# Performance work log

Measured on AMD Instinct MI355X. Metric: run time of the kernel, lower is better.

The kernel has to match this reference:

```python
import jax, jax.numpy as jnp
import numpy as np

B, T, C = 4, 2048, 1024
N_HEAD = 16
HEAD_DIM = C // N_HEAD


def setup_inputs() -> dict:
    key = jax.random.key(0)
    k1, k2, k3 = jax.random.split(key, 3)
    x = jax.random.normal(k1, (B, T, C), dtype=jnp.float32)
    # Linear weights stored as (in, out); scaled like typical init
    w_qkv = jax.random.normal(k2, (C, 3 * C), dtype=jnp.float32) * (1.0 / np.sqrt(C))
    w_proj = jax.random.normal(k3, (C, C), dtype=jnp.float32) * (1.0 / np.sqrt(C))
    return {"x": x, "w_qkv": w_qkv, "w_proj": w_proj}


def reference(x, w_qkv, w_proj):
    b, t, c = x.shape
    qkv = x @ w_qkv                      # (B,T,3C)
    q, k, v = jnp.split(qkv, 3, axis=-1)
    # (B,H,T,D)
    def to_heads(a):
        return a.reshape(b, t, N_HEAD, HEAD_DIM).transpose(0, 2, 1, 3)
    q, k, v = to_heads(q), to_heads(k), to_heads(v)
    scale = 1.0 / np.sqrt(HEAD_DIM).astype(np.float32)
    att = jnp.einsum('bhqd,bhkd->bhqk', q, k) * scale   # (B,H,T,T)
    causal = jnp.tril(jnp.ones((t, t), dtype=bool))
    att = jnp.where(causal[None, None, :, :], att, -jnp.inf)
    att = jax.nn.softmax(att, axis=-1)
    # dropout p=0.0 (eval) -> identity
    y = jnp.einsum('bhqk,bhkd->bhqd', att, v)            # (B,H,T,D)
    y = y.transpose(0, 2, 1, 3).reshape(b, t, c)
    return y @ w_proj
```

## Files before the change

### kernel.cpp

```cpp
#include <hip/hip_runtime.h>
#include <hip/hip_bf16.h>
#include <stdint.h>

#define Bsz 4
#define Tsz 2048
#define Csz 1024
#define Hn  16
#define Dh  64
#define BH  (Bsz*Hn)
#define Mrows (Bsz*Tsz)
#define N1  (3*Csz)

typedef short s16x8 __attribute__((ext_vector_type(8)));
typedef short s16x4 __attribute__((ext_vector_type(4)));
typedef float fx4   __attribute__((ext_vector_type(4)));

static __device__ __forceinline__ short f2bf(float x) {
  __hip_bfloat16 h = __float2bfloat16(x);
  return __builtin_bit_cast(short, h);
}

#define GLDS16(g, l) __builtin_amdgcn_global_load_lds( \
    (const __attribute__((address_space(1))) void*)(g), \
    (__attribute__((address_space(3))) void*)(l), 16, 0, 0)

__global__ void cvt_kernel(const float* __restrict__ in, short* __restrict__ out, int n4) {
  int i = blockIdx.x * blockDim.x + threadIdx.x;
  int stride = blockDim.x * gridDim.x;
  for (; i < n4; i += stride) {
    float4 v = ((const float4*)in)[i];
    s16x4 o;
    o.x = f2bf(v.x); o.y = f2bf(v.y); o.z = f2bf(v.z); o.w = f2bf(v.w);
    ((s16x4*)out)[i] = o;
  }
}

__global__ void transpose_cvt_kernel(const float* __restrict__ w, short* __restrict__ wt,
                                     int K, int N) {
  __shared__ float tile[32][33];
  int tc = threadIdx.x & 31;
  int tr = threadIdx.x >> 5;
  int n0 = blockIdx.x * 32;
  int k0 = blockIdx.y * 32;
#pragma unroll
  for (int p = 0; p < 4; p++) {
    int r = tr + p*8;
    tile[r][tc] = w[(size_t)(k0 + r) * N + (n0 + tc)];
  }
  __syncthreads();
#pragma unroll
  for (int p = 0; p < 4; p++) {
    int r = tr + p*8;
    wt[(size_t)(n0 + r) * K + (k0 + tc)] = f2bf(tile[tc][r]);
  }
}

static __device__ __forceinline__ void gemm_stage(
    const short* __restrict__ Ab, const short* __restrict__ Bb, int Kdim, int k0,
    short* __restrict__ sA, short* __restrict__ sB, int tid)
{
#pragma unroll
  for (int i = 0; i < 2; i++) {
    int c  = tid + 256*i;
    int mr = c >> 3;
    int l  = (c & 7) ^ (mr & 7);
    int row = mr*2 + (l >> 2);
    int ko  = (l & 3) * 8;
    GLDS16(Ab + (size_t)row * Kdim + k0 + ko, sA + c*8);
    GLDS16(Bb + (size_t)row * Kdim + k0 + ko, sB + c*8);
  }
}

static __device__ __forceinline__ void gemm_compute(
    const short* __restrict__ sA, const short* __restrict__ sB,
    int m_off, int n_off, int lr, int lq, fx4 acc[4][4])
{
  s16x8 af[4], bf[4];
#pragma unroll
  for (int mt = 0; mt < 4; mt++) {
    int m = m_off + mt*16 + lr, mr = m >> 1;
    int p = (((m & 1)*4 + lq)) ^ (mr & 7);
    af[mt] = *(const s16x8*)(sA + mr*64 + p*8);
  }
#pragma unroll
  for (int nt = 0; nt < 4; nt++) {
    int n = n_off + nt*16 + lr, nr = n >> 1;
    int p = (((n & 1)*4 + lq)) ^ (nr & 7);
    bf[nt] = *(const s16x8*)(sB + nr*64 + p*8);
  }
#pragma unroll
  for (int mt = 0; mt < 4; mt++)
#pragma unroll
    for (int nt = 0; nt < 4; nt++)
      acc[mt][nt] = __builtin_amdgcn_mfma_f32_16x16x32_bf16(af[mt], bf[nt], acc[mt][nt], 0, 0, 0);
}

__global__ __launch_bounds__(256) void gemm_bt_kernel(
    const short* __restrict__ A, const short* __restrict__ Bt,
    float* __restrict__ Cf,
    short* __restrict__ Qo, short* __restrict__ Ko, short* __restrict__ Vo,
    int Mdim, int Ndim, int Kdim, int mode)
{
  __shared__ __align__(16) short sA[2][128*32];
  __shared__ __align__(16) short sB[2][128*32];
  const int tid  = threadIdx.x;
  const int lane = tid & 63;
  const int lr   = lane & 15;
  const int lq   = lane >> 4;
  const int wv   = tid >> 6;
  const int nb   = Ndim >> 7;
  const int bm   = (int)blockIdx.x / nb;
  const int bn   = (int)blockIdx.x % nb;
  const int m_off = (wv & 1) << 6;
  const int n_off = (wv >> 1) << 6;

  const short* Ab = A  + (size_t)bm * 128 * Kdim;
  const short* Bb = Bt + (size_t)bn * 128 * Kdim;

  fx4 acc[4][4];
#pragma unroll
  for (int i = 0; i < 4; i++)
#pragma unroll
    for (int j = 0; j < 4; j++) acc[i][j] = (fx4){0.f, 0.f, 0.f, 0.f};

  const int NIT = Kdim >> 5;
  gemm_stage(Ab, Bb, Kdim, 0, sA[0], sB[0], tid);
  for (int it = 0; it < NIT; it += 2) {
    __syncthreads();
    if (it + 1 < NIT) gemm_stage(Ab, Bb, Kdim, (it+1)*32, sA[1], sB[1], tid);
    gemm_compute(sA[0], sB[0], m_off, n_off, lr, lq, acc);
    __syncthreads();
    if (it + 2 < NIT) gemm_stage(Ab, Bb, Kdim, (it+2)*32, sA[0], sB[0], tid);
    gemm_compute(sA[1], sB[1], m_off, n_off, lr, lq, acc);
  }

  const int gm0 = bm*128 + m_off;
  const int gn0 = bn*128 + n_off;
  if (mode == 0) {
#pragma unroll
    for (int mt = 0; mt < 4; mt++)
#pragma unroll
      for (int nt = 0; nt < 4; nt++) {
        int col = gn0 + nt*16 + lr;
#pragma unroll
        for (int r = 0; r < 4; r++) {
          int row = gm0 + mt*16 + lq*4 + r;
          Cf[(size_t)row * Ndim + col] = acc[mt][nt][r];
        }
      }
  } else {
#pragma unroll
    for (int mt = 0; mt < 4; mt++)
#pragma unroll
      for (int nt = 0; nt < 4; nt++) {
        int n   = gn0 + nt*16 + lr;
        int sec = n >> 10;
        int cc  = n & 1023;
        int hh  = cc >> 6;
        int dd  = cc & 63;
        if (sec == 2) {
          int tt0 = gm0 + mt*16 + lq*4;
          int bb  = tt0 >> 11;
          int bh  = bb * Hn + hh;
          s16x4 pk;
          pk.x = f2bf(acc[mt][nt][0]); pk.y = f2bf(acc[mt][nt][1]);
          pk.z = f2bf(acc[mt][nt][2]); pk.w = f2bf(acc[mt][nt][3]);
          *(s16x4*)(Vo + ((size_t)bh * Dh + dd) * Tsz + (tt0 & 2047)) = pk;
        } else {
#pragma unroll
          for (int r = 0; r < 4; r++) {
            int m  = gm0 + mt*16 + lq*4 + r;
            int bb = m >> 11;
            int tt = m & 2047;
            int bh = bb * Hn + hh;
            short v = f2bf(acc[mt][nt][r]);
            if (sec == 0) Qo[((size_t)bh * Tsz + tt) * Dh + dd] = v;
            else          Ko[((size_t)bh * Tsz + tt) * Dh + dd] = v;
          }
        }
      }
  }
}

#define PPITCH 72

static __device__ __forceinline__ void attn_stage(
    const short* __restrict__ Kp, const short* __restrict__ Vp, int kbase,
    short* __restrict__ sK, short* __restrict__ sV,
    int c0, int r0, int g0, int c1, int r1, int g1)
{
  GLDS16(Kp + (size_t)(kbase + r0)*Dh + g0, sK + c0*8);
  GLDS16(Kp + (size_t)(kbase + r1)*Dh + g1, sK + c1*8);
  GLDS16(Vp + (size_t)r0*Tsz + kbase + g0, sV + c0*8);
  GLDS16(Vp + (size_t)r1*Tsz + kbase + g1, sV + c1*8);
}

static __device__ __forceinline__ void attn_compute(
    const short* __restrict__ sK, const short* __restrict__ sV,
    int kbase, int q0, int lr, int lq, int sw,
    short* __restrict__ pb, const s16x8 bq[2][2], fx4 o[2][4], float li[2])
{
  const float sc = 0.125f * 1.44269504f;
  const bool masked = (kbase + 63 > q0);

  fx4 s[2][4];
#pragma unroll
  for (int j = 0; j < 2; j++)
#pragma unroll
    for (int mt = 0; mt < 4; mt++) s[j][mt] = (fx4){0.f,0.f,0.f,0.f};
#pragma unroll
  for (int mt = 0; mt < 4; mt++)
#pragma unroll
    for (int kk = 0; kk < 2; kk++) {
      const s16x8 akf = *(const s16x8*)(sK + (mt*16 + lr)*64 + ((kk*4 + lq) ^ sw)*8);
      s[0][mt] = __builtin_amdgcn_mfma_f32_16x16x32_bf16(akf, bq[0][kk], s[0][mt], 0, 0, 0);
      s[1][mt] = __builtin_amdgcn_mfma_f32_16x16x32_bf16(akf, bq[1][kk], s[1][mt], 0, 0, 0);
    }

#pragma unroll
  for (int j = 0; j < 2; j++) {
    const int qg = q0 + 16*j + lr;
    float p[16];
#pragma unroll
    for (int mt = 0; mt < 4; mt++)
#pragma unroll
      for (int r = 0; r < 4; r++) {
        float v = s[j][mt][r];
        if (masked) {
          int jg = kbase + mt*16 + lq*4 + r;
          v = (jg <= qg) ? v : -1e30f;
        }
        p[mt*4 + r] = __builtin_amdgcn_exp2f(v * sc);
      }
    float s8[8];
#pragma unroll
    for (int i = 0; i < 8; i++) s8[i] = p[i] + p[i+8];
    float s4[4];
#pragma unroll
    for (int i = 0; i < 4; i++) s4[i] = s8[i] + s8[i+4];
    li[j] += (s4[0] + s4[2]) + (s4[1] + s4[3]);
#pragma unroll
    for (int mt = 0; mt < 4; mt++) {
      s16x4 pk;
      pk.x = f2bf(p[mt*4+0]); pk.y = f2bf(p[mt*4+1]);
      pk.z = f2bf(p[mt*4+2]); pk.w = f2bf(p[mt*4+3]);
      *(s16x4*)(pb + (16*j + lr)*PPITCH + mt*16 + lq*4) = pk;
    }
  }
  __asm__ __volatile__("" ::: "memory");
  s16x8 pf[2][2];
#pragma unroll
  for (int j = 0; j < 2; j++)
#pragma unroll
    for (int kk = 0; kk < 2; kk++)
      pf[j][kk] = *(const s16x8*)(pb + (16*j + lr)*PPITCH + kk*32 + lq*8);
  __asm__ __volatile__("" ::: "memory");

#pragma unroll
  for (int dt = 0; dt < 4; dt++)
#pragma unroll
    for (int kk = 0; kk < 2; kk++) {
      const s16x8 avf = *(const s16x8*)(sV + (dt*16 + lr)*64 + ((kk*4 + lq) ^ sw)*8);
      o[0][dt] = __builtin_amdgcn_mfma_f32_16x16x32_bf16(avf, pf[0][kk], o[0][dt], 0, 0, 0);
      o[1][dt] = __builtin_amdgcn_mfma_f32_16x16x32_bf16(avf, pf[1][kk], o[1][dt], 0, 0, 0);
    }
}

__global__ __launch_bounds__(256) void attn_kernel(
    const short* __restrict__ Qb, const short* __restrict__ Kb,
    const short* __restrict__ Vt, short* __restrict__ Y)
{
  __shared__ __align__(16) short sK[2][64*64];
  __shared__ __align__(16) short sV[2][64*64];
  __shared__ __align__(16) short pbuf[4][32*PPITCH];
  const int tid  = threadIdx.x;
  const int lane = tid & 63;
  const int wv   = tid >> 6;
  const int lr   = lane & 15;
  const int lq   = lane >> 4;
  const int sw   = lr & 7;
  const int bh   = blockIdx.x;
  const int qb   = 15 - (int)blockIdx.y;
  const int b    = bh >> 4;
  const int h    = bh & 15;
  const int q0   = qb*128 + wv*32;

  const short* Qp = Qb + (size_t)bh * Tsz * Dh;
  const short* Kp = Kb + (size_t)bh * Tsz * Dh;
  const short* Vp = Vt + (size_t)bh * Dh * Tsz;
  short* pb = pbuf[wv];

  const int c0 = tid,       r0 = c0 >> 3, g0 = (((c0 & 7) ^ (r0 & 7)) * 8);
  const int c1 = tid + 256, r1 = c1 >> 3, g1 = (((c1 & 7) ^ (r1 & 7)) * 8);

  s16x8 bq[2][2];
#pragma unroll
  for (int j = 0; j < 2; j++)
#pragma unroll
    for (int kk = 0; kk < 2; kk++)
      bq[j][kk] = *(const s16x8*)(Qp + (size_t)(q0 + 16*j + lr)*Dh + kk*32 + lq*8);

  fx4 o[2][4];
#pragma unroll
  for (int j = 0; j < 2; j++)
#pragma unroll
    for (int i = 0; i < 4; i++) o[j][i] = (fx4){0.f, 0.f, 0.f, 0.f};
  float li[2] = {0.f, 0.f};

  const int ntiles = 2*qb + 2;
  attn_stage(Kp, Vp, 0, sK[0], sV[0], c0, r0, g0, c1, r1, g1);
  for (int kt = 0; kt < ntiles; kt += 2) {
    __syncthreads();
    if (kt + 1 < ntiles) attn_stage(Kp, Vp, (kt+1)*64, sK[1], sV[1], c0, r0, g0, c1, r1, g1);
    if (kt*64 <= q0 + 31)
      attn_compute(sK[0], sV[0], kt*64, q0, lr, lq, sw, pb, bq, o, li);
    __syncthreads();
    if (kt + 2 < ntiles) attn_stage(Kp, Vp, (kt+2)*64, sK[0], sV[0], c0, r0, g0, c1, r1, g1);
    if ((kt+1)*64 <= q0 + 31)
      attn_compute(sK[1], sV[1], (kt+1)*64, q0, lr, lq, sw, pb, bq, o, li);
  }

#pragma unroll
  for (int j = 0; j < 2; j++) {
    float l = li[j];
    l += __shfl_xor(l, 16);
    l += __shfl_xor(l, 32);
    float inv = 1.0f / l;
#pragma unroll
    for (int dt = 0; dt < 4; dt++) {
      s16x4 yk;
      yk.x = f2bf(o[j][dt][0]*inv); yk.y = f2bf(o[j][dt][1]*inv);
      yk.z = f2bf(o[j][dt][2]*inv); yk.w = f2bf(o[j][dt][3]*inv);
      *(s16x4*)(Y + ((size_t)b*Tsz + q0 + 16*j + lr)*Csz + h*Dh + dt*16 + lq*4) = yk;
    }
  }
}

extern "C" void kernel_launch(void* const* d_in, const int* in_sizes, int n_in,
                              void* d_out, int out_size, void* d_ws, size_t ws_size,
                              hipStream_t stream)
{
  const float* x  = (const float*)d_in[0];
  const float* wq = (const float*)d_in[1];
  const float* wp = (const float*)d_in[2];
  float* out = (float*)d_out;

  char* ws = (char*)d_ws;
  size_t off = 0;
  short* xb  = (short*)(ws + off); off += (size_t)Mrows*Csz*2;
  short* wqT = (short*)(ws + off); off += (size_t)N1*Csz*2;
  short* wpT = (short*)(ws + off); off += (size_t)Csz*Csz*2;
  short* Qb  = (short*)(ws + off); off += (size_t)BH*Tsz*Dh*2;
  short* Kb  = (short*)(ws + off); off += (size_t)BH*Tsz*Dh*2;
  short* Vt  = (short*)(ws + off); off += (size_t)BH*Dh*Tsz*2;
  short* Yb  = (short*)(ws + off); off += (size_t)Mrows*Csz*2;

  cvt_kernel<<<1024, 256, 0, stream>>>(x, xb, Mrows*Csz/4);
  transpose_cvt_kernel<<<dim3(N1/32, Csz/32), 256, 0, stream>>>(wq, wqT, Csz, N1);
  transpose_cvt_kernel<<<dim3(Csz/32, Csz/32), 256, 0, stream>>>(wp, wpT, Csz, Csz);
  gemm_bt_kernel<<<(Mrows/128)*(N1/128), 256, 0, stream>>>(
      xb, wqT, nullptr, Qb, Kb, Vt, Mrows, N1, Csz, 1);
  attn_kernel<<<dim3(BH, Tsz/128), 256, 0, stream>>>(Qb, Kb, Vt, Yb);
  gemm_bt_kernel<<<(Mrows/128)*(Csz/128), 256, 0, stream>>>(
      Yb, wpT, out, nullptr, nullptr, nullptr, Mrows, Csz, Csz, 0);
}
```

Before: 263.2 us.

## Restructure GEMM into 128x256 tiles with triple-buffered LDS pipeline

The bf16 GEMM now uses 512-thread blocks computing 128x256 output tiles with a K step of 64. LDS staging is triple-buffered, with explicit vmcnt waits so global->LDS loads for stage t+2 overlap the MFMAs of stage t. MFMA clusters are split into two halves separated by barriers and wrapped in s_setprio, and swizzled LDS offsets are precomputed once. This is meant to cut barrier and load latency and raise MFMA utilisation, at the cost of more LDS per block (144 KB), which lowers occupancy, and fewer blocks in the grid.

```diff
diff --git a/kernel.cpp b/kernel.cpp
--- a/kernel.cpp
+++ b/kernel.cpp
@@ -55,67 +55,55 @@
   }
 }
 
-static __device__ __forceinline__ void gemm_stage(
-    const short* __restrict__ Ab, const short* __restrict__ Bb, int Kdim, int k0,
-    short* __restrict__ sA, short* __restrict__ sB, int tid)
-{
-#pragma unroll
-  for (int i = 0; i < 2; i++) {
-    int c  = tid + 256*i;
-    int mr = c >> 3;
-    int l  = (c & 7) ^ (mr & 7);
-    int row = mr*2 + (l >> 2);
-    int ko  = (l & 3) * 8;
-    GLDS16(Ab + (size_t)row * Kdim + k0 + ko, sA + c*8);
-    GLDS16(Bb + (size_t)row * Kdim + k0 + ko, sB + c*8);
-  }
-}
-
-static __device__ __forceinline__ void gemm_compute(
-    const short* __restrict__ sA, const short* __restrict__ sB,
-    int m_off, int n_off, int lr, int lq, fx4 acc[4][4])
-{
-  s16x8 af[4], bf[4];
-#pragma unroll
-  for (int mt = 0; mt < 4; mt++) {
-    int m = m_off + mt*16 + lr, mr = m >> 1;
-    int p = (((m & 1)*4 + lq)) ^ (mr & 7);
-    af[mt] = *(const s16x8*)(sA + mr*64 + p*8);
-  }
-#pragma unroll
-  for (int nt = 0; nt < 4; nt++) {
-    int n = n_off + nt*16 + lr, nr = n >> 1;
-    int p = (((n & 1)*4 + lq)) ^ (nr & 7);
-    bf[nt] = *(const s16x8*)(sB + nr*64 + p*8);
-  }
-#pragma unroll
-  for (int mt = 0; mt < 4; mt++)
-#pragma unroll
-    for (int nt = 0; nt < 4; nt++)
-      acc[mt][nt] = __builtin_amdgcn_mfma_f32_16x16x32_bf16(af[mt], bf[nt], acc[mt][nt], 0, 0, 0);
-}
-
-__global__ __launch_bounds__(256) void gemm_bt_kernel(
+static __device__ __forceinline__ s16x8 lds_frag(const short* p, int off) {
+  return *(const s16x8*)(p + off);
+}
+
+__global__ __launch_bounds__(512) void gemm_bt_kernel(
     const short* __restrict__ A, const short* __restrict__ Bt,
     float* __restrict__ Cf,
     short* __restrict__ Qo, short* __restrict__ Ko, short* __restrict__ Vo,
     int Mdim, int Ndim, int Kdim, int mode)
 {
-  __shared__ __align__(16) short sA[2][128*32];
-  __shared__ __align__(16) short sB[2][128*32];
+  __shared__ __align__(16) short sA[3][128*64];
+  __shared__ __align__(16) short sB[3][256*64];
   const int tid  = threadIdx.x;
   const int lane = tid & 63;
   const int lr   = lane & 15;
   const int lq   = lane >> 4;
   const int wv   = tid >> 6;
-  const int nb   = Ndim >> 7;
+  const int nb   = Ndim >> 8;
   const int bm   = (int)blockIdx.x / nb;
   const int bn   = (int)blockIdx.x % nb;
   const int m_off = (wv & 1) << 6;
   const int n_off = (wv >> 1) << 6;
 
   const short* Ab = A  + (size_t)bm * 128 * Kdim;
-  const short* Bb = Bt + (size_t)bn * 128 * Kdim;
+  const short* Bb = Bt + (size_t)bn * 256 * Kdim;
+
+  const short* gA[2];
+  const short* gB[4];
+#pragma unroll
+  for (int j = 0; j < 2; j++) {
+    int c = tid + 512*j, r = c >> 3, o = ((c & 7) ^ (r & 7)) * 8;
+    gA[j] = Ab + (size_t)r * Kdim + o;
+  }
+#pragma unroll
+  for (int j = 0; j < 4; j++) {
+    int c = tid + 512*j, r = c >> 3, o = ((c & 7) ^ (r & 7)) * 8;
+    gB[j] = Bb + (size_t)r * Kdim + o;
+  }
+
+  int offA[4][2], offB[4][2];
+#pragma unroll
+  for (int ft = 0; ft < 4; ft++)
+#pragma unroll
+    for (int kk = 0; kk < 2; kk++) {
+      int ra = m_off + ft*16 + lr;
+      offA[ft][kk] = ra*64 + ((((kk<<2) | lq) ^ (ra & 7)) << 3);
+      int rb = n_off + ft*16 + lr;
+      offB[ft][kk] = rb*64 + ((((kk<<2) | lq) ^ (rb & 7)) << 3);
+    }
 
   fx4 acc[4][4];
 #pragma unroll
@@ -123,19 +111,82 @@
 #pragma unroll
     for (int j = 0; j < 4; j++) acc[i][j] = (fx4){0.f, 0.f, 0.f, 0.f};
 
-  const int NIT = Kdim >> 5;
-  gemm_stage(Ab, Bb, Kdim, 0, sA[0], sB[0], tid);
-  for (int it = 0; it < NIT; it += 2) {
-    __syncthreads();
-    if (it + 1 < NIT) gemm_stage(Ab, Bb, Kdim, (it+1)*32, sA[1], sB[1], tid);
-    gemm_compute(sA[0], sB[0], m_off, n_off, lr, lq, acc);
-    __syncthreads();
-    if (it + 2 < NIT) gemm_stage(Ab, Bb, Kdim, (it+2)*32, sA[0], sB[0], tid);
-    gemm_compute(sA[1], sB[1], m_off, n_off, lr, lq, acc);
+  auto STAGE = [&](int k0, short* dA, short* dB) {
+    GLDS16(gA[0] + k0, dA + tid*8);
+    GLDS16(gA[1] + k0, dA + (tid+512)*8);
+    GLDS16(gB[0] + k0, dB + tid*8);
+    GLDS16(gB[1] + k0, dB + (tid+512)*8);
+    GLDS16(gB[2] + k0, dB + (tid+1024)*8);
+    GLDS16(gB[3] + k0, dB + (tid+1536)*8);
+  };
+
+  const int NIT = Kdim >> 6;
+
+  STAGE(0,  sA[0], sB[0]);
+  STAGE(64, sA[1], sB[1]);
+  __asm__ __volatile__("s_waitcnt vmcnt(6)" ::: "memory");
+  __builtin_amdgcn_s_barrier();
+
+  const short *cA = sA[0], *cB = sB[0];
+  const short *nA = sA[1], *nB = sB[1];
+  short *eA = sA[2], *eB = sB[2];
+
+  for (int t = 0; t < NIT; ++t) {
+    if (t + 2 < NIT) STAGE((t+2)*64, eA, eB);
+
+    s16x8 af[4][2], bf[2][2];
+#pragma unroll
+    for (int mt = 0; mt < 4; mt++)
+#pragma unroll
+      for (int kk = 0; kk < 2; kk++)
+        af[mt][kk] = lds_frag(cA, offA[mt][kk]);
+#pragma unroll
+    for (int nt = 0; nt < 2; nt++)
+#pragma unroll
+      for (int kk = 0; kk < 2; kk++)
+        bf[nt][kk] = lds_frag(cB, offB[nt][kk]);
+    __builtin_amdgcn_s_setprio(1);
+#pragma unroll
+    for (int kk = 0; kk < 2; kk++)
+#pragma unroll
+      for (int mt = 0; mt < 4; mt++) {
+        acc[mt][0] = __builtin_amdgcn_mfma_f32_16x16x32_bf16(af[mt][kk], bf[0][kk], acc[mt][0], 0, 0, 0);
+        acc[mt][1] = __builtin_amdgcn_mfma_f32_16x16x32_bf16(af[mt][kk], bf[1][kk], acc[mt][1], 0, 0, 0);
+      }
+    __builtin_amdgcn_s_setprio(0);
+    __builtin_amdgcn_sched_barrier(0);
+    __builtin_amdgcn_s_barrier();
+
+#pragma unroll
+    for (int nt = 0; nt < 2; nt++)
+#pragma unroll
+      for (int kk = 0; kk < 2; kk++)
+        bf[nt][kk] = lds_frag(cB, offB[nt+2][kk]);
+    __builtin_amdgcn_s_setprio(1);
+#pragma unroll
+    for (int kk = 0; kk < 2; kk++)
+#pragma unroll
+      for (int mt = 0; mt < 4; mt++) {
+        acc[mt][2] = __builtin_amdgcn_mfma_f32_16x16x32_bf16(af[mt][kk], bf[0][kk], acc[mt][2], 0, 0, 0);
+        acc[mt][3] = __builtin_amdgcn_mfma_f32_16x16x32_bf16(af[mt][kk], bf[1][kk], acc[mt][3], 0, 0, 0);
+      }
+    __builtin_amdgcn_s_setprio(0);
+    __builtin_amdgcn_sched_barrier(0);
+    if (t + 2 < NIT) {
+      __asm__ __volatile__("s_waitcnt vmcnt(6)" ::: "memory");
+    } else if (t + 1 < NIT) {
+      __asm__ __volatile__("s_waitcnt vmcnt(0)" ::: "memory");
+    }
+    __builtin_amdgcn_s_barrier();
+
+    const short *tAp = cA, *tBp = cB;
+    cA = nA; cB = nB;
+    nA = eA; nB = eB;
+    eA = (short*)tAp; eB = (short*)tBp;
   }
 
   const int gm0 = bm*128 + m_off;
-  const int gn0 = bn*128 + n_off;
+  const int gn0 = bn*256 + n_off;
   if (mode == 0) {
 #pragma unroll
     for (int mt = 0; mt < 4; mt++)
@@ -358,9 +409,9 @@
   cvt_kernel<<<1024, 256, 0, stream>>>(x, xb, Mrows*Csz/4);
   transpose_cvt_kernel<<<dim3(N1/32, Csz/32), 256, 0, stream>>>(wq, wqT, Csz, N1);
   transpose_cvt_kernel<<<dim3(Csz/32, Csz/32), 256, 0, stream>>>(wp, wpT, Csz, Csz);
-  gemm_bt_kernel<<<(Mrows/128)*(N1/128), 256, 0, stream>>>(
+  gemm_bt_kernel<<<(Mrows/128)*(N1/256), 512, 0, stream>>>(
       xb, wqT, nullptr, Qb, Kb, Vt, Mrows, N1, Csz, 1);
   attn_kernel<<<dim3(BH, Tsz/128), 256, 0, stream>>>(Qb, Kb, Vt, Yb);
-  gemm_bt_kernel<<<(Mrows/128)*(Csz/128), 256, 0, stream>>>(
+  gemm_bt_kernel<<<(Mrows/128)*(Csz/256), 512, 0, stream>>>(
       Yb, wpT, out, nullptr, nullptr, nullptr, Mrows, Csz, Csz, 0);
 }
```

After: 261.1 us. No clear change (-0.8%).
